# Kernel optimization log

Hardware: AMD Instinct MI355X
Metric: run time of the kernel (lower is better)

The kernel has to match this reference:

```python
import jax, jax.numpy as jnp
import numpy as np

N_NODES = 50000
N_HEDGES = 50000
NNZ = 800000
F_IN, HID, OUT = 256, 256, 128


def setup_inputs() -> dict:
    key = jax.random.key(0)
    ks = jax.random.split(key, 8)
    x = jax.random.normal(ks[0], (N_NODES, F_IN), dtype=jnp.float32)
    vi = jax.random.randint(ks[1], (NNZ,), 0, N_NODES)
    hi = jax.random.randint(ks[2], (NNZ,), 0, N_HEDGES)
    edge_index = jnp.stack([vi, hi], axis=0).astype(jnp.int64)
    edge_weight = jnp.ones((NNZ,), dtype=jnp.float32)
    # glorot-ish init for the v2e linear weights; e2v bias zeros (bias_e2v=True)
    W1 = jax.random.normal(ks[3], (F_IN, HID), dtype=jnp.float32) / np.sqrt(F_IN)
    b1 = jnp.zeros((HID,), dtype=jnp.float32)
    W2 = jax.random.normal(ks[4], (HID, HID), dtype=jnp.float32) / np.sqrt(HID)
    b2 = jnp.zeros((HID,), dtype=jnp.float32)
    W3 = jax.random.normal(ks[5], (HID, OUT), dtype=jnp.float32) / np.sqrt(HID)
    b3 = jnp.zeros((OUT,), dtype=jnp.float32)
    return {"x": x, "edge_index": edge_index, "edge_weight": edge_weight,
            "W1": W1, "b1": b1, "W2": W2, "b2": b2, "W3": W3, "b3": b3}


def _conv(x, vi, hi, deg_v, deg_e, W, b):
    """HNN_general_conv: linear (weight_v2e) -> mean scatter v->e -> mean scatter e->v + bias (bias_e2v)."""
    msg = x @ W                                             # [N, C]
    xe = jax.ops.segment_sum(msg[vi], hi, num_segments=N_HEDGES) / deg_e  # [E, C]
    xv = jax.ops.segment_sum(xe[hi], vi, num_segments=N_NODES) / deg_v + b  # [N, C]
    return xv, xe


def reference(x, edge_index, edge_weight, W1, b1, W2, b2, W3, b3):
    vi = edge_index[0].astype(jnp.int32)
    hi = edge_index[1].astype(jnp.int32)
    ones = jnp.ones((NNZ,), dtype=x.dtype)
    deg_v = jnp.maximum(jax.ops.segment_sum(ones, vi, num_segments=N_NODES), 1.0)[:, None]
    deg_e = jnp.maximum(jax.ops.segment_sum(ones, hi, num_segments=N_HEDGES), 1.0)[:, None]
    # layer 1 and 2: conv -> ELU (dropout is identity in eval mode)
    h, _ = _conv(x, vi, hi, deg_v, deg_e, W1, b1)
    h = jax.nn.elu(h)
    h, _ = _conv(h, vi, hi, deg_v, deg_e, W2, b2)
    h = jax.nn.elu(h)
    # last layer: no activation
    out, _ = _conv(h, vi, hi, deg_v, deg_e, W3, b3)
    return out
```

## Files before the change

### kernel.cpp

```cpp
#include <hip/hip_runtime.h>
#include <math.h>

#define NN 50000
#define NE 50000
#define NNZ_E 800000
#define NBUCK 196
#define BCAP 8192
#define EPB 2048

typedef _Float16 half_t;
typedef half_t half8 __attribute__((ext_vector_type(8)));
typedef half_t half4v __attribute__((ext_vector_type(4)));
typedef float floatx4 __attribute__((ext_vector_type(4)));
typedef float floatx8 __attribute__((ext_vector_type(8)));


__global__ __launch_bounds__(256) void bin_kernel(const int* __restrict__ vi,
                                                  const int* __restrict__ hi,
                                                  int* __restrict__ bcur_e,
                                                  int* __restrict__ bcur_v,
                                                  unsigned int* __restrict__ tmp_e,
                                                  unsigned int* __restrict__ tmp_v) {
    __shared__ int cnt_e[NBUCK], cnt_v[NBUCK];
    __shared__ int gb_e[NBUCK], gb_v[NBUCK];
    int tid = threadIdx.x;
    for (int i = tid; i < NBUCK; i += 256) { cnt_e[i] = 0; cnt_v[i] = 0; }
    __syncthreads();
    int base = blockIdx.x * EPB;
    int nE = NNZ_E - base; if (nE > EPB) nE = EPB;
    int v[8], e[8], re[8], rv[8];
#pragma unroll
    for (int i = 0; i < 8; i++) {
        int off = i * 256 + tid;
        if (off < nE) {
            int k = base + off;
            v[i] = vi[k]; e[i] = hi[k];
            re[i] = atomicAdd(&cnt_e[e[i] >> 8], 1);
            rv[i] = atomicAdd(&cnt_v[v[i] >> 8], 1);
        }
    }
    __syncthreads();
    for (int i = tid; i < NBUCK; i += 256) {
        if (cnt_e[i] > 0) gb_e[i] = atomicAdd(&bcur_e[i], cnt_e[i]);
        if (cnt_v[i] > 0) gb_v[i] = atomicAdd(&bcur_v[i], cnt_v[i]);
    }
    __syncthreads();
#pragma unroll
    for (int i = 0; i < 8; i++) {
        int off = i * 256 + tid;
        if (off < nE) {
            int be = e[i] >> 8, bv = v[i] >> 8;
            tmp_e[(size_t)be * BCAP + gb_e[be] + re[i]] = ((unsigned)v[i] << 8) | (e[i] & 255);
            tmp_v[(size_t)bv * BCAP + gb_v[bv] + rv[i]] = ((unsigned)e[i] << 8) | (v[i] & 255);
        }
    }
}

__global__ __launch_bounds__(256) void fine_count(const int* __restrict__ bcur,
                                                  const unsigned int* __restrict__ tmp,
                                                  int* __restrict__ counts, int nseg) {
    __shared__ int h[256];
    int b = blockIdx.x, tid = threadIdx.x;
    h[tid] = 0;
    __syncthreads();
    int n = bcur[b];
    const unsigned int* t = tmp + (size_t)b * BCAP;
    for (int i = tid; i < n; i += 256) atomicAdd(&h[t[i] & 255], 1);
    __syncthreads();
    int seg = b * 256 + tid;
    if (seg < nseg) counts[seg] = h[tid];
}

__global__ __launch_bounds__(256) void fine_scatter(const int* __restrict__ bcur,
                                                    const unsigned int* __restrict__ tmp,
                                                    const int* __restrict__ offs,
                                                    int* __restrict__ payload, int nseg) {
    __shared__ int cur[256];
    int b = blockIdx.x, tid = threadIdx.x;
    int seg = b * 256 + tid;
    cur[tid] = (seg < nseg) ? offs[seg] : 0;
    __syncthreads();
    int n = bcur[b];
    const unsigned int* t = tmp + (size_t)b * BCAP;
    for (int i = tid; i < n; i += 256) {
        unsigned int r = t[i];
        int pos = atomicAdd(&cur[r & 255], 1);
        payload[pos] = r >> 8;
    }
}


__global__ __launch_bounds__(256) void scan_blk(const int* __restrict__ counts,
                                                int* __restrict__ offs,
                                                int* __restrict__ blocksum, int n) {
    __shared__ int sh[256];
    int tid = threadIdx.x;
    int i = blockIdx.x * 256 + tid;
    int v = (i < n) ? counts[i] : 0;
    sh[tid] = v;
    __syncthreads();
    for (int o = 1; o < 256; o <<= 1) {
        int add = (tid >= o) ? sh[tid - o] : 0;
        __syncthreads();
        sh[tid] += add;
        __syncthreads();
    }
    if (i < n) offs[i] = sh[tid] - v;
    if (tid == 255) blocksum[blockIdx.x] = sh[255];
}

__global__ __launch_bounds__(256) void scan_top(const int* __restrict__ blocksum,
                                                int* __restrict__ blockbase, int nb) {
    __shared__ int sh[256];
    int tid = threadIdx.x;
    int v = (tid < nb) ? blocksum[tid] : 0;
    sh[tid] = v;
    __syncthreads();
    for (int o = 1; o < 256; o <<= 1) {
        int add = (tid >= o) ? sh[tid - o] : 0;
        __syncthreads();
        sh[tid] += add;
        __syncthreads();
    }
    if (tid < nb) blockbase[tid] = sh[tid] - v;
}

__global__ void scan_fix(const int* __restrict__ counts, const int* __restrict__ blockbase,
                         int* __restrict__ offs, float* __restrict__ inv, int n) {
    int i = blockIdx.x * 256 + threadIdx.x;
    if (i < n) {
        offs[i] = offs[i] + blockbase[i >> 8];
        inv[i] = 1.0f / fmaxf((float)counts[i], 1.0f);
    }
}


__global__ void cvt_split(const float* __restrict__ X, half_t* __restrict__ Xh,
                          half_t* __restrict__ Xl, int nrows) {
    int i = (blockIdx.x * 256 + threadIdx.x) * 4;
    if (i < nrows * 256) {
        float4 v = *(const float4*)(X + i);
        half4v h, l;
        h.x = (half_t)v.x; l.x = (half_t)(v.x - (float)h.x);
        h.y = (half_t)v.y; l.y = (half_t)(v.y - (float)h.y);
        h.z = (half_t)v.z; l.z = (half_t)(v.z - (float)h.z);
        h.w = (half_t)v.w; l.w = (half_t)(v.w - (float)h.w);
        int row = i >> 8, ch = i & 255;
        size_t di = (size_t)(ch >> 5) * nrows * 32 + (size_t)row * 32 + (ch & 31);
        *(half4v*)(Xh + di) = h;
        *(half4v*)(Xl + di) = l;
    }
}

__global__ void cvt_w(const float* __restrict__ W, half_t* __restrict__ Wth,
                      half_t* __restrict__ Wtl, int Kd, int Nd) {
    int idx = blockIdx.x * 256 + threadIdx.x;
    if (idx < Kd * Nd) {
        int k = idx / Nd, n = idx - k * Nd;
        float v = W[idx];
        half_t h = (half_t)v;
        Wth[(size_t)n * Kd + k] = h;
        Wtl[(size_t)n * Kd + k] = (half_t)(v - (float)h);
    }
}


#define LSTR 40

__global__ __launch_bounds__(256) void gemm_hsplit(const half_t* __restrict__ Ah,
                                                   const half_t* __restrict__ Al,
                                                   const half_t* __restrict__ Bh,
                                                   const half_t* __restrict__ Bl,
                                                   half_t* __restrict__ C,
                                                   int M, int N, int K) {
    __shared__ __attribute__((aligned(16))) half_t sAh[128 * LSTR];
    __shared__ __attribute__((aligned(16))) half_t sAl[128 * LSTR];
    __shared__ __attribute__((aligned(16))) half_t sBh[128 * LSTR];
    __shared__ __attribute__((aligned(16))) half_t sBl[128 * LSTR];

    int tid = threadIdx.x;
    int wave = tid >> 6, lane = tid & 63;
    int row0 = blockIdx.y * 128, col0 = blockIdx.x * 128;
    int qm = (wave >> 1) * 64, qn = (wave & 1) * 64;

    int sr = tid >> 1;
    int sk = (tid & 1) * 16;
    int fm = lane & 15;
    int fk = (lane >> 4) * 8;

    floatx4 acc[4][4] = {};

    for (int k0 = 0; k0 < K; k0 += 32) {
        half8 a0 = {}, a1 = {}, l0 = {}, l1 = {};
        int arow = row0 + sr;
        int kk = k0 + sk;
        if (arow < M) {
            size_t ai = (size_t)(kk >> 5) * M * 32 + (size_t)arow * 32 + (kk & 31);
            a0 = *(const half8*)(Ah + ai); a1 = *(const half8*)(Ah + ai + 8);
            l0 = *(const half8*)(Al + ai); l1 = *(const half8*)(Al + ai + 8);
        }
        *(half8*)&sAh[sr * LSTR + sk]     = a0;
        *(half8*)&sAh[sr * LSTR + sk + 8] = a1;
        *(half8*)&sAl[sr * LSTR + sk]     = l0;
        *(half8*)&sAl[sr * LSTR + sk + 8] = l1;
        {
            const half_t* pb = Bh + (size_t)(col0 + sr) * K + k0 + sk;
            const half_t* pc = Bl + (size_t)(col0 + sr) * K + k0 + sk;
            half8 b0 = *(const half8*)pb, b1 = *(const half8*)(pb + 8);
            half8 c0 = *(const half8*)pc, c1 = *(const half8*)(pc + 8);
            *(half8*)&sBh[sr * LSTR + sk]     = b0;
            *(half8*)&sBh[sr * LSTR + sk + 8] = b1;
            *(half8*)&sBl[sr * LSTR + sk]     = c0;
            *(half8*)&sBl[sr * LSTR + sk + 8] = c1;
        }
        __syncthreads();

        half8 fa_h[4], fa_l[4], fb_h[4], fb_l[4];
#pragma unroll
        for (int i = 0; i < 4; i++) {
            fa_h[i] = *(const half8*)&sAh[(qm + i * 16 + fm) * LSTR + fk];
            fa_l[i] = *(const half8*)&sAl[(qm + i * 16 + fm) * LSTR + fk];
            fb_h[i] = *(const half8*)&sBh[(qn + i * 16 + fm) * LSTR + fk];
            fb_l[i] = *(const half8*)&sBl[(qn + i * 16 + fm) * LSTR + fk];
        }
#pragma unroll
        for (int mi = 0; mi < 4; mi++)
#pragma unroll
            for (int ni = 0; ni < 4; ni++) {
                acc[mi][ni] = __builtin_amdgcn_mfma_f32_16x16x32_f16(fa_h[mi], fb_h[ni], acc[mi][ni], 0, 0, 0);
                acc[mi][ni] = __builtin_amdgcn_mfma_f32_16x16x32_f16(fa_h[mi], fb_l[ni], acc[mi][ni], 0, 0, 0);
                acc[mi][ni] = __builtin_amdgcn_mfma_f32_16x16x32_f16(fa_l[mi], fb_h[ni], acc[mi][ni], 0, 0, 0);
            }
        __syncthreads();
    }

    int er = (lane >> 4) * 4;
    int ec = lane & 15;
#pragma unroll
    for (int mi = 0; mi < 4; mi++)
#pragma unroll
        for (int r = 0; r < 4; r++) {
            int grow = row0 + qm + mi * 16 + er + r;
            if (grow < M) {
#pragma unroll
                for (int ni = 0; ni < 4; ni++) {
                    int col = col0 + qn + ni * 16 + ec;
                    size_t ci = (size_t)(col >> 5) * M * 32 + (size_t)grow * 32 + (col & 31);
                    __builtin_nontemporal_store((half_t)acc[mi][ni][r], C + ci);
                }
            }
        }
}


template <int NCHUNK, int MODE>
__global__ __launch_bounds__(256) void seg16(const half_t* __restrict__ src,
                                             const int* __restrict__ offs,
                                             const int* __restrict__ counts,
                                             const int* __restrict__ payload,
                                             const float* __restrict__ inv,
                                             const float* __restrict__ bias,
                                             half_t* __restrict__ dst_h,
                                             half_t* __restrict__ dst_l,
                                             float* __restrict__ dst_f,
                                             int nrows, int nsrc) {
    int chunk = blockIdx.x % NCHUNK;
    int grp = blockIdx.x / NCHUNK;
    int tid = threadIdx.x;
    int row = grp * 64 + (tid >> 2);
    if (row >= nrows) return;
    int co = (tid & 3) * 8;
    const half_t* sbase = src + (size_t)chunk * nsrc * 32 + co;
    int start = offs[row], cnt = counts[row];
    int j = start, end = start + cnt;
    floatx8 a0 = {}, a1 = {}, a2 = {}, a3 = {};
    for (; j + 4 <= end; j += 4) {
        int s0 = __builtin_nontemporal_load(payload + j);
        int s1 = __builtin_nontemporal_load(payload + j + 1);
        int s2 = __builtin_nontemporal_load(payload + j + 2);
        int s3 = __builtin_nontemporal_load(payload + j + 3);
        half8 v0 = *(const half8*)(sbase + (size_t)s0 * 32);
        half8 v1 = *(const half8*)(sbase + (size_t)s1 * 32);
        half8 v2 = *(const half8*)(sbase + (size_t)s2 * 32);
        half8 v3 = *(const half8*)(sbase + (size_t)s3 * 32);
        a0 += __builtin_convertvector(v0, floatx8);
        a1 += __builtin_convertvector(v1, floatx8);
        a2 += __builtin_convertvector(v2, floatx8);
        a3 += __builtin_convertvector(v3, floatx8);
    }
    for (; j < end; j++) {
        int sr = __builtin_nontemporal_load(payload + j);
        half8 v = *(const half8*)(sbase + (size_t)sr * 32);
        a0 += __builtin_convertvector(v, floatx8);
    }
    floatx8 acc = (a0 + a1) + (a2 + a3);
    acc *= inv[row];
    int gch = chunk * 32 + co;
    if (MODE >= 1) {
        float4 b0 = *(const float4*)(bias + gch);
        float4 b1 = *(const float4*)(bias + gch + 4);
        acc[0] += b0.x; acc[1] += b0.y; acc[2] += b0.z; acc[3] += b0.w;
        acc[4] += b1.x; acc[5] += b1.y; acc[6] += b1.z; acc[7] += b1.w;
    }
    if (MODE == 1) {
#pragma unroll
        for (int k = 0; k < 8; k++) acc[k] = acc[k] > 0.f ? acc[k] : expm1f(acc[k]);
        half8 h = __builtin_convertvector(acc, half8);
        floatx8 back = __builtin_convertvector(h, floatx8);
        half8 l = __builtin_convertvector(acc - back, half8);
        size_t di = (size_t)chunk * nrows * 32 + (size_t)row * 32 + co;
        __builtin_nontemporal_store(h, (half8*)(dst_h + di));
        __builtin_nontemporal_store(l, (half8*)(dst_l + di));
    } else if (MODE == 0) {
        size_t di = (size_t)chunk * nrows * 32 + (size_t)row * 32 + co;
        __builtin_nontemporal_store(__builtin_convertvector(acc, half8), (half8*)(dst_h + di));
    } else {
        float* o = dst_f + (size_t)row * (NCHUNK * 32) + gch;
        floatx4 lo = {acc[0], acc[1], acc[2], acc[3]};
        floatx4 hi4 = {acc[4], acc[5], acc[6], acc[7]};
        __builtin_nontemporal_store(lo, (floatx4*)o);
        __builtin_nontemporal_store(hi4, (floatx4*)(o + 4));
    }
}


extern "C" void kernel_launch(void* const* d_in, const int* in_sizes, int n_in,
                              void* d_out, int out_size, void* d_ws, size_t ws_size,
                              hipStream_t stream) {
    const float* x  = (const float*)d_in[0];
    const int*   ei = (const int*)d_in[1];
    const int* vi = ei;
    const int* hi = ei + NNZ_E;
    const float* W1 = (const float*)d_in[3];
    const float* b1 = (const float*)d_in[4];
    const float* W2 = (const float*)d_in[5];
    const float* b2 = (const float*)d_in[6];
    const float* W3 = (const float*)d_in[7];
    const float* b3 = (const float*)d_in[8];
    float* out = (float*)d_out;

    char* p = (char*)d_ws;
    auto take = [&](size_t bytes) -> void* {
        void* r = (void*)p;
        p += (bytes + 255) & ~(size_t)255;
        return r;
    };
    const int NB = (NN + 255) / 256;
    int* counts_v = (int*)take(NN * 4);
    int* counts_e = (int*)take(NE * 4);
    int* offs_v   = (int*)take(NN * 4);
    int* offs_e   = (int*)take(NE * 4);
    int* bsum_v   = (int*)take(NB * 4);
    int* bsum_e   = (int*)take(NB * 4);
    int* bbase_v  = (int*)take(NB * 4);
    int* bbase_e  = (int*)take(NB * 4);
    int* bcur_e   = (int*)take(NBUCK * 4);
    int* bcur_v   = (int*)take(NBUCK * 4);
    unsigned int* tmp_e = (unsigned int*)take((size_t)NBUCK * BCAP * 4);
    unsigned int* tmp_v = (unsigned int*)take((size_t)NBUCK * BCAP * 4);
    int* pay_v    = (int*)take((size_t)NNZ_E * 4);
    int* pay_e    = (int*)take((size_t)NNZ_E * 4);
    float* inv_v  = (float*)take(NN * 4);
    float* inv_e  = (float*)take(NE * 4);
    half_t* msgH  = (half_t*)take((size_t)NN * 256 * 2);
    half_t* xeH   = (half_t*)take((size_t)NE * 256 * 2);
    half_t* hA_h  = (half_t*)take((size_t)NN * 256 * 2);
    half_t* hA_l  = (half_t*)take((size_t)NN * 256 * 2);
    half_t* w1h   = (half_t*)take(256 * 256 * 2);
    half_t* w1l   = (half_t*)take(256 * 256 * 2);
    half_t* w2h   = (half_t*)take(256 * 256 * 2);
    half_t* w2l   = (half_t*)take(256 * 256 * 2);
    half_t* w3h   = (half_t*)take(256 * 128 * 2);
    half_t* w3l   = (half_t*)take(256 * 128 * 2);

    hipMemsetAsync(bcur_e, 0, NBUCK * 4, stream);
    hipMemsetAsync(bcur_v, 0, NBUCK * 4, stream);
    bin_kernel<<<(NNZ_E + EPB - 1) / EPB, 256, 0, stream>>>(vi, hi, bcur_e, bcur_v, tmp_e, tmp_v);
    fine_count<<<NBUCK, 256, 0, stream>>>(bcur_e, tmp_e, counts_e, NE);
    fine_count<<<NBUCK, 256, 0, stream>>>(bcur_v, tmp_v, counts_v, NN);
    scan_blk<<<NB, 256, 0, stream>>>(counts_v, offs_v, bsum_v, NN);
    scan_blk<<<NB, 256, 0, stream>>>(counts_e, offs_e, bsum_e, NE);
    scan_top<<<1, 256, 0, stream>>>(bsum_v, bbase_v, NB);
    scan_top<<<1, 256, 0, stream>>>(bsum_e, bbase_e, NB);
    scan_fix<<<NB, 256, 0, stream>>>(counts_v, bbase_v, offs_v, inv_v, NN);
    scan_fix<<<NB, 256, 0, stream>>>(counts_e, bbase_e, offs_e, inv_e, NE);
    fine_scatter<<<NBUCK, 256, 0, stream>>>(bcur_e, tmp_e, offs_e, pay_e, NE);
    fine_scatter<<<NBUCK, 256, 0, stream>>>(bcur_v, tmp_v, offs_v, pay_v, NN);

    cvt_split<<<(NN * 256 / 4 + 255) / 256, 256, 0, stream>>>(x, hA_h, hA_l, NN);
    cvt_w<<<(256 * 256 + 255) / 256, 256, 0, stream>>>(W1, w1h, w1l, 256, 256);
    cvt_w<<<(256 * 256 + 255) / 256, 256, 0, stream>>>(W2, w2h, w2l, 256, 256);
    cvt_w<<<(256 * 128 + 255) / 256, 256, 0, stream>>>(W3, w3h, w3l, 256, 128);

    dim3 g256(2, (NN + 127) / 128);
    dim3 g128(1, (NN + 127) / 128);
    int grpN = (NN + 63) / 64;
    int gridC256 = 8 * grpN;
    int gridC128 = 4 * grpN;

    gemm_hsplit<<<g256, 256, 0, stream>>>(hA_h, hA_l, w1h, w1l, msgH, NN, 256, 256);
    seg16<8, 0><<<gridC256, 256, 0, stream>>>(msgH, offs_e, counts_e, pay_e, inv_e,
                                              nullptr, xeH, nullptr, nullptr, NE, NN);
    seg16<8, 1><<<gridC256, 256, 0, stream>>>(xeH, offs_v, counts_v, pay_v, inv_v,
                                              b1, hA_h, hA_l, nullptr, NN, NE);
    gemm_hsplit<<<g256, 256, 0, stream>>>(hA_h, hA_l, w2h, w2l, msgH, NN, 256, 256);
    seg16<8, 0><<<gridC256, 256, 0, stream>>>(msgH, offs_e, counts_e, pay_e, inv_e,
                                              nullptr, xeH, nullptr, nullptr, NE, NN);
    seg16<8, 1><<<gridC256, 256, 0, stream>>>(xeH, offs_v, counts_v, pay_v, inv_v,
                                              b2, hA_h, hA_l, nullptr, NN, NE);
    gemm_hsplit<<<g128, 256, 0, stream>>>(hA_h, hA_l, w3h, w3l, msgH, NN, 128, 256);
    seg16<4, 0><<<gridC128, 256, 0, stream>>>(msgH, offs_e, counts_e, pay_e, inv_e,
                                              nullptr, xeH, nullptr, nullptr, NE, NN);
    seg16<4, 2><<<gridC128, 256, 0, stream>>>(xeH, offs_v, counts_v, pay_v, inv_v,
                                              b3, nullptr, nullptr, out, NN, NE);
}
```

Measured before the change: 699.6 us.

## Sort segment rows by degree for balanced waves and unroll gather to 8

```diff
diff --git a/kernel.cpp b/kernel.cpp
--- a/kernel.cpp
+++ b/kernel.cpp
@@ -131,6 +131,37 @@
     if (i < n) {
         offs[i] = offs[i] + blockbase[i >> 8];
         inv[i] = 1.0f / fmaxf((float)counts[i], 1.0f);
+    }
+}
+
+
+__global__ void hist256(const int* __restrict__ counts, int* __restrict__ hist, int n) {
+    int i = blockIdx.x * 256 + threadIdx.x;
+    if (i < n) atomicAdd(&hist[min(counts[i], 255)], 1);
+}
+
+__global__ __launch_bounds__(256) void hist_scan(const int* __restrict__ hist,
+                                                 int* __restrict__ cursor) {
+    __shared__ int sh[256];
+    int tid = threadIdx.x;
+    int v = hist[tid];
+    sh[tid] = v;
+    __syncthreads();
+    for (int o = 1; o < 256; o <<= 1) {
+        int add = (tid >= o) ? sh[tid - o] : 0;
+        __syncthreads();
+        sh[tid] += add;
+        __syncthreads();
+    }
+    cursor[tid] = sh[tid] - v;
+}
+
+__global__ void order_scatter(const int* __restrict__ counts, int* __restrict__ cursor,
+                              int* __restrict__ order, int n) {
+    int i = blockIdx.x * 256 + threadIdx.x;
+    if (i < n) {
+        int pos = atomicAdd(&cursor[min(counts[i], 255)], 1);
+        order[pos] = i;
     }
 }
 
@@ -255,6 +286,7 @@
 
 template <int NCHUNK, int MODE>
 __global__ __launch_bounds__(256) void seg16(const half_t* __restrict__ src,
+                                             const int* __restrict__ order,
                                              const int* __restrict__ offs,
                                              const int* __restrict__ counts,
                                              const int* __restrict__ payload,
@@ -267,13 +299,41 @@
     int chunk = blockIdx.x % NCHUNK;
     int grp = blockIdx.x / NCHUNK;
     int tid = threadIdx.x;
-    int row = grp * 64 + (tid >> 2);
-    if (row >= nrows) return;
+    int idx = grp * 64 + (tid >> 2);
+    if (idx >= nrows) return;
+    int row = order[idx];
     int co = (tid & 3) * 8;
     const half_t* sbase = src + (size_t)chunk * nsrc * 32 + co;
     int start = offs[row], cnt = counts[row];
     int j = start, end = start + cnt;
     floatx8 a0 = {}, a1 = {}, a2 = {}, a3 = {};
+    floatx8 a4 = {}, a5 = {}, a6 = {}, a7 = {};
+    for (; j + 8 <= end; j += 8) {
+        int s0 = __builtin_nontemporal_load(payload + j);
+        int s1 = __builtin_nontemporal_load(payload + j + 1);
+        int s2 = __builtin_nontemporal_load(payload + j + 2);
+        int s3 = __builtin_nontemporal_load(payload + j + 3);
+        int s4 = __builtin_nontemporal_load(payload + j + 4);
+        int s5 = __builtin_nontemporal_load(payload + j + 5);
+        int s6 = __builtin_nontemporal_load(payload + j + 6);
+        int s7 = __builtin_nontemporal_load(payload + j + 7);
+        half8 v0 = *(const half8*)(sbase + (size_t)s0 * 32);
+        half8 v1 = *(const half8*)(sbase + (size_t)s1 * 32);
+        half8 v2 = *(const half8*)(sbase + (size_t)s2 * 32);
+        half8 v3 = *(const half8*)(sbase + (size_t)s3 * 32);
+        half8 v4 = *(const half8*)(sbase + (size_t)s4 * 32);
+        half8 v5 = *(const half8*)(sbase + (size_t)s5 * 32);
+        half8 v6 = *(const half8*)(sbase + (size_t)s6 * 32);
+        half8 v7 = *(const half8*)(sbase + (size_t)s7 * 32);
+        a0 += __builtin_convertvector(v0, floatx8);
+        a1 += __builtin_convertvector(v1, floatx8);
+        a2 += __builtin_convertvector(v2, floatx8);
+        a3 += __builtin_convertvector(v3, floatx8);
+        a4 += __builtin_convertvector(v4, floatx8);
+        a5 += __builtin_convertvector(v5, floatx8);
+        a6 += __builtin_convertvector(v6, floatx8);
+        a7 += __builtin_convertvector(v7, floatx8);
+    }
     for (; j + 4 <= end; j += 4) {
         int s0 = __builtin_nontemporal_load(payload + j);
         int s1 = __builtin_nontemporal_load(payload + j + 1);
@@ -293,7 +353,7 @@
         half8 v = *(const half8*)(sbase + (size_t)sr * 32);
         a0 += __builtin_convertvector(v, floatx8);
     }
-    floatx8 acc = (a0 + a1) + (a2 + a3);
+    floatx8 acc = ((a0 + a1) + (a2 + a3)) + ((a4 + a5) + (a6 + a7));
     acc *= inv[row];
     int gch = chunk * 32 + co;
     if (MODE >= 1) {
@@ -356,6 +416,12 @@
     int* bbase_e  = (int*)take(NB * 4);
     int* bcur_e   = (int*)take(NBUCK * 4);
     int* bcur_v   = (int*)take(NBUCK * 4);
+    int* hist_v   = (int*)take(256 * 4);
+    int* hist_e   = (int*)take(256 * 4);
+    int* hcur_v   = (int*)take(256 * 4);
+    int* hcur_e   = (int*)take(256 * 4);
+    int* order_v  = (int*)take(NN * 4);
+    int* order_e  = (int*)take(NE * 4);
     unsigned int* tmp_e = (unsigned int*)take((size_t)NBUCK * BCAP * 4);
     unsigned int* tmp_v = (unsigned int*)take((size_t)NBUCK * BCAP * 4);
     int* pay_v    = (int*)take((size_t)NNZ_E * 4);
@@ -375,6 +441,8 @@
 
     hipMemsetAsync(bcur_e, 0, NBUCK * 4, stream);
     hipMemsetAsync(bcur_v, 0, NBUCK * 4, stream);
+    hipMemsetAsync(hist_v, 0, 256 * 4, stream);
+    hipMemsetAsync(hist_e, 0, 256 * 4, stream);
     bin_kernel<<<(NNZ_E + EPB - 1) / EPB, 256, 0, stream>>>(vi, hi, bcur_e, bcur_v, tmp_e, tmp_v);
     fine_count<<<NBUCK, 256, 0, stream>>>(bcur_e, tmp_e, counts_e, NE);
     fine_count<<<NBUCK, 256, 0, stream>>>(bcur_v, tmp_v, counts_v, NN);
@@ -387,6 +455,13 @@
     fine_scatter<<<NBUCK, 256, 0, stream>>>(bcur_e, tmp_e, offs_e, pay_e, NE);
     fine_scatter<<<NBUCK, 256, 0, stream>>>(bcur_v, tmp_v, offs_v, pay_v, NN);
 
+    hist256<<<NB, 256, 0, stream>>>(counts_v, hist_v, NN);
+    hist256<<<NB, 256, 0, stream>>>(counts_e, hist_e, NE);
+    hist_scan<<<1, 256, 0, stream>>>(hist_v, hcur_v);
+    hist_scan<<<1, 256, 0, stream>>>(hist_e, hcur_e);
+    order_scatter<<<NB, 256, 0, stream>>>(counts_v, hcur_v, order_v, NN);
+    order_scatter<<<NB, 256, 0, stream>>>(counts_e, hcur_e, order_e, NE);
+
     cvt_split<<<(NN * 256 / 4 + 255) / 256, 256, 0, stream>>>(x, hA_h, hA_l, NN);
     cvt_w<<<(256 * 256 + 255) / 256, 256, 0, stream>>>(W1, w1h, w1l, 256, 256);
     cvt_w<<<(256 * 256 + 255) / 256, 256, 0, stream>>>(W2, w2h, w2l, 256, 256);
@@ -399,18 +474,18 @@
     int gridC128 = 4 * grpN;
 
     gemm_hsplit<<<g256, 256, 0, stream>>>(hA_h, hA_l, w1h, w1l, msgH, NN, 256, 256);
-    seg16<8, 0><<<gridC256, 256, 0, stream>>>(msgH, offs_e, counts_e, pay_e, inv_e,
+    seg16<8, 0><<<gridC256, 256, 0, stream>>>(msgH, order_e, offs_e, counts_e, pay_e, inv_e,
                                               nullptr, xeH, nullptr, nullptr, NE, NN);
-    seg16<8, 1><<<gridC256, 256, 0, stream>>>(xeH, offs_v, counts_v, pay_v, inv_v,
+    seg16<8, 1><<<gridC256, 256, 0, stream>>>(xeH, order_v, offs_v, counts_v, pay_v, inv_v,
                                               b1, hA_h, hA_l, nullptr, NN, NE);
     gemm_hsplit<<<g256, 256, 0, stream>>>(hA_h, hA_l, w2h, w2l, msgH, NN, 256, 256);
-    seg16<8, 0><<<gridC256, 256, 0, stream>>>(msgH, offs_e, counts_e, pay_e, inv_e,
+    seg16<8, 0><<<gridC256, 256, 0, stream>>>(msgH, order_e, offs_e, counts_e, pay_e, inv_e,
                                               nullptr, xeH, nullptr, nullptr, NE, NN);
-    seg16<8, 1><<<gridC256, 256, 0, stream>>>(xeH, offs_v, counts_v, pay_v, inv_v,
+    seg16<8, 1><<<gridC256, 256, 0, stream>>>(xeH, order_v, offs_v, counts_v, pay_v, inv_v,
                                               b2, hA_h, hA_l, nullptr, NN, NE);
     gemm_hsplit<<<g128, 256, 0, stream>>>(hA_h, hA_l, w3h, w3l, msgH, NN, 128, 256);
-    seg16<4, 0><<<gridC128, 256, 0, stream>>>(msgH, offs_e, counts_e, pay_e, inv_e,
+    seg16<4, 0><<<gridC128, 256, 0, stream>>>(msgH, order_e, offs_e, counts_e, pay_e, inv_e,
                                               nullptr, xeH, nullptr, nullptr, NE, NN);
-    seg16<4, 2><<<gridC128, 256, 0, stream>>>(xeH, offs_v, counts_v, pay_v, inv_v,
+    seg16<4, 2><<<gridC128, 256, 0, stream>>>(xeH, order_v, offs_v, counts_v, pay_v, inv_v,
                                               b3, nullptr, nullptr, out, NN, NE);
 }
```

Result: slower. 1.325 ms (+89.4%).
